# Performance work log

Hardware: AMD Instinct MI355X
Metric: run time of the kernel (lower is better)

Reference implementation:

```python
import jax, jax.numpy as jnp
import numpy as np

B, S, N, D, H, C, E, DG = 2, 512, 20000, 384, 3, 128, 320000, 128
NEG_SLOPE = 0.2  # PyG GATConv default


def setup_inputs() -> dict:
    key = jax.random.key(0)
    ks = jax.random.split(key, 10)
    p = lambda k, sh: jax.random.normal(k, sh, jnp.float32) * 0.02
    return dict(
        x_enc=jax.random.normal(ks[0], (B, S, D), jnp.float32),
        mask=jax.random.uniform(ks[1], (B, N), dtype=jnp.float32),
        edge_index=jax.random.randint(ks[2], (2, E), 0, N),
        Wq=p(ks[3], (N, S)), bq=jnp.zeros((N,), jnp.float32),
        Wm=p(ks[4], (D, 1)), bm=jnp.zeros((D,), jnp.float32),
        Wlin=p(ks[5], (H * C, D)),
        att_src=p(ks[6], (H, C)), att_dst=p(ks[7], (H, C)),
        bias_gat=jnp.zeros((H * C,), jnp.float32),
        Wproj=p(ks[8], (S, N)), bproj=jnp.zeros((S,), jnp.float32),
        Wtemp=p(ks[9], (DG, H * C)), btemp=jnp.zeros((DG,), jnp.float32),
    )


def reference(x_enc, mask, edge_index, Wq, bq, Wm, bm, Wlin, att_src, att_dst,
              bias_gat, Wproj, bproj, Wtemp, btemp):
    # q = query_proj(x_enc.permute(0,2,1)).permute(0,2,1)  -> [B, N, D]
    q = jnp.einsum('bsd,ns->bnd', x_enc, Wq) + bq[None, :, None]
    # mask_proj: Linear(1, D) on mask[..., None]  -> [B, N, D]
    mask_embed = mask[..., None] * Wm[:, 0] + bm
    x = (q + mask_embed).reshape(B * N, D)

    # batch edge_index with per-graph node offsets, then add self-loops (PyG default)
    offs = (jnp.arange(B, dtype=edge_index.dtype) * N)[:, None]
    src = (edge_index[0][None, :] + offs).reshape(-1)
    dst = (edge_index[1][None, :] + offs).reshape(-1)
    loops = jnp.arange(B * N, dtype=edge_index.dtype)
    src = jnp.concatenate([src, loops])
    dst = jnp.concatenate([dst, loops])

    # GATConv: shared linear, per-head attention
    xp = (x @ Wlin.T).reshape(B * N, H, C)                  # [BN, H, C]
    a_src = jnp.einsum('nhc,hc->nh', xp, att_src)           # [BN, H]
    a_dst = jnp.einsum('nhc,hc->nh', xp, att_dst)
    e = jax.nn.leaky_relu(a_src[src] + a_dst[dst], NEG_SLOPE)  # [Etot, H]
    # segment-softmax over incoming edges of each destination node
    emax = jax.ops.segment_max(e, dst, num_segments=B * N)
    ee = jnp.exp(e - emax[dst])
    denom = jax.ops.segment_sum(ee, dst, num_segments=B * N)
    alpha = ee / denom[dst]                                  # [Etot, H]
    out = jax.ops.segment_sum(xp[src] * alpha[..., None], dst, num_segments=B * N)
    out = out.reshape(B, N, H * C) + bias_gat                # concat heads + bias

    # dropout is identity in eval
    # project: Linear(N, S) over node dim -> [B, S, H*C]
    out = jnp.einsum('bnf,sn->bsf', out, Wproj) + bproj[None, :, None]
    # temp_project: Linear(H*C, d_graph)
    out = out @ Wtemp.T + btemp
    return out
```

## Files before the change

### kernel.cpp

```cpp
#include <hip/hip_runtime.h>
#include <hip/hip_bf16.h>
#include <cstdint>

#define B_   2
#define S_   512
#define N_   20000
#define H_   3
#define C_   128
#define E_   320000
#define DG_  128
#define D_   384
#define BN_  (B_ * N_)
#define F_   (H_ * C_)
#define ETOT_ (B_ * E_ + BN_)

#define MPADQ 20096
#define MPADL 40064

#define PNS2 32
#define PCH2 640

using short8  = __attribute__((ext_vector_type(8))) short;
using floatx4 = __attribute__((ext_vector_type(4))) float;

__device__ __forceinline__ float b2f(unsigned short u) {
  union { unsigned int i; float f; } x; x.i = ((unsigned int)u) << 16; return x.f;
}
__device__ __forceinline__ unsigned short f2b(float f) {
  __hip_bfloat16 b = __float2bfloat16(f);
  return *reinterpret_cast<unsigned short*>(&b);
}

struct bf4 { __hip_bfloat16 a, b, c, d; };

__global__ __launch_bounds__(256) void conv_wq_kernel(const float* __restrict__ Wq,
                                                      __hip_bfloat16* __restrict__ o) {
  int idx = blockIdx.x * 256 + threadIdx.x;
  if (idx >= (MPADQ * 512) / 4) return;
  int e = idx * 4;
  int row = e >> 9;
  float4 v = make_float4(0.f, 0.f, 0.f, 0.f);
  if (row < N_) v = *(const float4*)(Wq + e);
  bf4 r{__float2bfloat16(v.x), __float2bfloat16(v.y),
        __float2bfloat16(v.z), __float2bfloat16(v.w)};
  *(bf4*)(o + e) = r;
}

__global__ __launch_bounds__(256) void conv_bf16_kernel(const float* __restrict__ W,
                                                        __hip_bfloat16* __restrict__ o,
                                                        int n4) {
  int idx = blockIdx.x * 256 + threadIdx.x;
  if (idx >= n4) return;
  int e = idx * 4;
  float4 v = *(const float4*)(W + e);
  bf4 r{__float2bfloat16(v.x), __float2bfloat16(v.y),
        __float2bfloat16(v.z), __float2bfloat16(v.w)};
  *(bf4*)(o + e) = r;
}

__global__ __launch_bounds__(256) void prep_epi_kernel(
    const float* __restrict__ Wlin, const float* __restrict__ Wm,
    const float* __restrict__ bm, const float* __restrict__ Wtemp,
    float* __restrict__ epi, float* __restrict__ swt) {
  int w = (blockIdx.x * 256 + threadIdx.x) >> 6;
  int lane = threadIdx.x & 63;
  if (w < F_) {
    float s0 = 0.f, s1 = 0.f, s2 = 0.f;
    const float* row = Wlin + (size_t)w * D_;
    for (int d = lane; d < D_; d += 64) {
      float wv = row[d];
      s0 += wv; s1 += Wm[d] * wv; s2 += bm[d] * wv;
    }
#pragma unroll
    for (int o = 32; o > 0; o >>= 1) {
      s0 += __shfl_down(s0, o); s1 += __shfl_down(s1, o); s2 += __shfl_down(s2, o);
    }
    if (lane == 0) { epi[w] = s0; epi[F_ + w] = s1; epi[2 * F_ + w] = s2; }
  } else if (w < F_ + DG_) {
    int g = w - F_;
    float s = 0.f;
    const float* row = Wtemp + (size_t)g * F_;
    for (int f = lane; f < F_; f += 64) s += row[f];
#pragma unroll
    for (int o = 32; o > 0; o >>= 1) s += __shfl_down(s, o);
    if (lane == 0) swt[g] = s;
  }
}

template <int EPI>
__global__ __launch_bounds__(256) void mfma_gemm_nt(
    const __hip_bfloat16* __restrict__ A, const __hip_bfloat16* __restrict__ Bt,
    __hip_bfloat16* __restrict__ Cout, int K, int Mvalid, int ldc,
    size_t bstrideB, size_t bstrideC,
    const float* __restrict__ bq, const float* __restrict__ mask,
    const float* __restrict__ epi) {
  const int tid = threadIdx.x;
  const int m0 = blockIdx.x * 128;
  const int n0 = blockIdx.y * 128;
  const int bz = blockIdx.z;

  const unsigned short* Ap = (const unsigned short*)A;
  const unsigned short* Bp = (const unsigned short*)(Bt + bstrideB * bz);

  __shared__ __align__(16) unsigned short As[128][40];
  __shared__ __align__(16) unsigned short Bs[128][40];

  const int wave = tid >> 6, lane = tid & 63;
  const int wm = (wave & 1) * 64, wn = (wave >> 1) * 64;
  const int lrow = lane & 15, lk = (lane >> 4) * 8;

  const int srow = tid >> 2;
  const int skoff = (tid & 3) * 8;

  floatx4 acc[4][4];
#pragma unroll
  for (int i = 0; i < 4; ++i)
#pragma unroll
    for (int j = 0; j < 4; ++j) acc[i][j] = floatx4{0.f, 0.f, 0.f, 0.f};

  for (int k0 = 0; k0 < K; k0 += 32) {
    int4 av0 = *(const int4*)(Ap + (size_t)(m0 + srow) * K + k0 + skoff);
    int4 av1 = *(const int4*)(Ap + (size_t)(m0 + 64 + srow) * K + k0 + skoff);
    int4 bv0 = *(const int4*)(Bp + (size_t)(n0 + srow) * K + k0 + skoff);
    int4 bv1 = *(const int4*)(Bp + (size_t)(n0 + 64 + srow) * K + k0 + skoff);
    __syncthreads();
    *(int4*)&As[srow][skoff] = av0;
    *(int4*)&As[64 + srow][skoff] = av1;
    *(int4*)&Bs[srow][skoff] = bv0;
    *(int4*)&Bs[64 + srow][skoff] = bv1;
    __syncthreads();
    short8 af[4], bf[4];
#pragma unroll
    for (int mt = 0; mt < 4; ++mt)
      af[mt] = *(const short8*)&As[wm + mt * 16 + lrow][lk];
#pragma unroll
    for (int nt = 0; nt < 4; ++nt)
      bf[nt] = *(const short8*)&Bs[wn + nt * 16 + lrow][lk];
#pragma unroll
    for (int mt = 0; mt < 4; ++mt)
#pragma unroll
      for (int nt = 0; nt < 4; ++nt)
        acc[mt][nt] = __builtin_amdgcn_mfma_f32_16x16x32_bf16(af[mt], bf[nt],
                                                              acc[mt][nt], 0, 0, 0);
  }

  __hip_bfloat16* Cb = Cout + bstrideC * bz;
#pragma unroll
  for (int mt = 0; mt < 4; ++mt) {
#pragma unroll
    for (int r = 0; r < 4; ++r) {
      int rg = m0 + wm + mt * 16 + (lane >> 4) * 4 + r;
      if (rg < Mvalid) {
        float bqv = 0.f, mkv = 0.f;
        if (EPI) {
          bqv = bq[rg];
          mkv = mask[bz * N_ + rg];
        }
#pragma unroll
        for (int nt = 0; nt < 4; ++nt) {
          int cg = n0 + wn + nt * 16 + lrow;
          float v = acc[mt][nt][r];
          if (EPI) v += bqv * epi[cg] + mkv * epi[F_ + cg] + epi[2 * F_ + cg];
          Cb[(size_t)rg * ldc + cg] = __float2bfloat16(v);
        }
      }
    }
  }
}

__global__ __launch_bounds__(256) void gemm_gn(
    const __hip_bfloat16* __restrict__ A, const __hip_bfloat16* __restrict__ Bt,
    __hip_bfloat16* __restrict__ gnT) {
  const int tid = threadIdx.x;
  const int m0 = blockIdx.x * 128;

  const unsigned short* Ap = (const unsigned short*)A;
  const unsigned short* Bp = (const unsigned short*)Bt;

  __shared__ __align__(16) unsigned short As[128][40];
  __shared__ __align__(16) unsigned short Bs[128][40];

  const int wave = tid >> 6, lane = tid & 63;
  const int wm = (wave & 1) * 64, wn = (wave >> 1) * 64;
  const int lrow = lane & 15, lk = (lane >> 4) * 8;
  const int srow = tid >> 2;
  const int skoff = (tid & 3) * 8;

  floatx4 acc[4][4];
#pragma unroll
  for (int i = 0; i < 4; ++i)
#pragma unroll
    for (int j = 0; j < 4; ++j) acc[i][j] = floatx4{0.f, 0.f, 0.f, 0.f};

  for (int k0 = 0; k0 < F_; k0 += 32) {
    int4 av0 = *(const int4*)(Ap + (size_t)(m0 + srow) * F_ + k0 + skoff);
    int4 av1 = *(const int4*)(Ap + (size_t)(m0 + 64 + srow) * F_ + k0 + skoff);
    int4 bv0 = *(const int4*)(Bp + (size_t)(srow) * F_ + k0 + skoff);
    int4 bv1 = *(const int4*)(Bp + (size_t)(64 + srow) * F_ + k0 + skoff);
    __syncthreads();
    *(int4*)&As[srow][skoff] = av0;
    *(int4*)&As[64 + srow][skoff] = av1;
    *(int4*)&Bs[srow][skoff] = bv0;
    *(int4*)&Bs[64 + srow][skoff] = bv1;
    __syncthreads();
    short8 af[4], bf[4];
#pragma unroll
    for (int mt = 0; mt < 4; ++mt)
      af[mt] = *(const short8*)&As[wm + mt * 16 + lrow][lk];
#pragma unroll
    for (int nt = 0; nt < 4; ++nt)
      bf[nt] = *(const short8*)&Bs[wn + nt * 16 + lrow][lk];
#pragma unroll
    for (int mt = 0; mt < 4; ++mt)
#pragma unroll
      for (int nt = 0; nt < 4; ++nt)
        acc[mt][nt] = __builtin_amdgcn_mfma_f32_16x16x32_bf16(af[mt], bf[nt],
                                                              acc[mt][nt], 0, 0, 0);
  }

#pragma unroll
  for (int mt = 0; mt < 4; ++mt) {
    int rg0 = m0 + wm + mt * 16 + (lane >> 4) * 4;
    if (rg0 < BN_) {
      int b = (rg0 >= N_) ? 1 : 0;
      int n = rg0 - b * N_;
#pragma unroll
      for (int nt = 0; nt < 4; ++nt) {
        int cg = wn + nt * 16 + lrow;
        ushort4 o;
        o.x = f2b(acc[mt][nt][0]); o.y = f2b(acc[mt][nt][1]);
        o.z = f2b(acc[mt][nt][2]); o.w = f2b(acc[mt][nt][3]);
        *(ushort4*)((unsigned short*)gnT + (size_t)b * DG_ * N_ + (size_t)cg * N_ + n) = o;
      }
    }
  }
}

__global__ __launch_bounds__(256) void gemm_proj2(
    const __hip_bfloat16* __restrict__ A, const __hip_bfloat16* __restrict__ Bt,
    float* __restrict__ Ppart) {
  const int tid = threadIdx.x;
  const int m0 = blockIdx.x * 128;
  const int bz = blockIdx.z;
  const int b = bz / PNS2, ks = bz - b * PNS2;
  const int kbeg = ks * PCH2;
  const int kend = (kbeg + PCH2 < N_) ? (kbeg + PCH2) : N_;

  const unsigned short* Ap = (const unsigned short*)A;
  const unsigned short* Bp = (const unsigned short*)(Bt + (size_t)b * DG_ * N_);

  __shared__ __align__(16) unsigned short As[128][40];
  __shared__ __align__(16) unsigned short Bs[128][40];

  const int wave = tid >> 6, lane = tid & 63;
  const int wm = (wave & 1) * 64, wn = (wave >> 1) * 64;
  const int lrow = lane & 15, lk = (lane >> 4) * 8;
  const int srow = tid >> 2;
  const int skoff = (tid & 3) * 8;

  floatx4 acc[4][4];
#pragma unroll
  for (int i = 0; i < 4; ++i)
#pragma unroll
    for (int j = 0; j < 4; ++j) acc[i][j] = floatx4{0.f, 0.f, 0.f, 0.f};

  for (int k0 = kbeg; k0 < kend; k0 += 32) {
    int4 av0 = *(const int4*)(Ap + (size_t)(m0 + srow) * N_ + k0 + skoff);
    int4 av1 = *(const int4*)(Ap + (size_t)(m0 + 64 + srow) * N_ + k0 + skoff);
    int4 bv0 = *(const int4*)(Bp + (size_t)(srow) * N_ + k0 + skoff);
    int4 bv1 = *(const int4*)(Bp + (size_t)(64 + srow) * N_ + k0 + skoff);
    __syncthreads();
    *(int4*)&As[srow][skoff] = av0;
    *(int4*)&As[64 + srow][skoff] = av1;
    *(int4*)&Bs[srow][skoff] = bv0;
    *(int4*)&Bs[64 + srow][skoff] = bv1;
    __syncthreads();
    short8 af[4], bf[4];
#pragma unroll
    for (int mt = 0; mt < 4; ++mt)
      af[mt] = *(const short8*)&As[wm + mt * 16 + lrow][lk];
#pragma unroll
    for (int nt = 0; nt < 4; ++nt)
      bf[nt] = *(const short8*)&Bs[wn + nt * 16 + lrow][lk];
#pragma unroll
    for (int mt = 0; mt < 4; ++mt)
#pragma unroll
      for (int nt = 0; nt < 4; ++nt)
        acc[mt][nt] = __builtin_amdgcn_mfma_f32_16x16x32_bf16(af[mt], bf[nt],
                                                              acc[mt][nt], 0, 0, 0);
  }

  float* Pp = Ppart + (size_t)bz * S_ * DG_;
#pragma unroll
  for (int mt = 0; mt < 4; ++mt) {
#pragma unroll
    for (int r = 0; r < 4; ++r) {
      int rg = m0 + wm + mt * 16 + (lane >> 4) * 4 + r;
#pragma unroll
      for (int nt = 0; nt < 4; ++nt) {
        int cg = wn + nt * 16 + lrow;
        Pp[(size_t)rg * DG_ + cg] = acc[mt][nt][r];
      }
    }
  }
}

__global__ __launch_bounds__(256) void att_kernel(
    const __hip_bfloat16* __restrict__ xp, const float* __restrict__ att_src,
    const float* __restrict__ att_dst, float* __restrict__ a_src,
    float* __restrict__ a_dst) {
  int gid = blockIdx.x * blockDim.x + threadIdx.x;
  int wid = gid >> 6;
  int lane = threadIdx.x & 63;
  if (wid >= BN_ * H_) return;
  int i = wid / H_, h = wid - i * H_;
  const __hip_bfloat16* row = xp + (size_t)i * F_ + h * C_;
  const float* as = att_src + h * C_;
  const float* ad = att_dst + h * C_;
  float v0 = __bfloat162float(row[lane]), v1 = __bfloat162float(row[lane + 64]);
  float s1 = v0 * as[lane] + v1 * as[lane + 64];
  float s2 = v0 * ad[lane] + v1 * ad[lane + 64];
#pragma unroll
  for (int off = 32; off > 0; off >>= 1) {
    s1 += __shfl_down(s1, off);
    s2 += __shfl_down(s2, off);
  }
  if (lane == 0) {
    a_src[i * H_ + h] = s1;
    a_dst[i * H_ + h] = s2;
  }
}

__global__ __launch_bounds__(256) void count_kernel(const int* __restrict__ ei,
                                                    int* __restrict__ counts,
                                                    int* __restrict__ rank) {
  int idx = blockIdx.x * blockDim.x + threadIdx.x;
  if (idx >= 2 * E_) return;
  int b = (idx >= E_) ? 1 : 0;
  int e = idx - b * E_;
  int d = ei[E_ + e];
  rank[idx] = atomicAdd(&counts[b * N_ + d], 1);
}

__global__ __launch_bounds__(1024) void scan_kernel(const int* __restrict__ counts,
                                                    int* __restrict__ offs) {
  __shared__ int wsum[16];
  __shared__ int carry;
  int t = threadIdx.x, wave = t >> 6, lane = t & 63;
  if (t == 0) carry = 0;
  __syncthreads();
  for (int base = 0; base < BN_; base += 1024) {
    int i = base + t;
    int v = (i < BN_) ? (counts[i] + 1) : 0;
    int x = v;
#pragma unroll
    for (int o = 1; o < 64; o <<= 1) {
      int y = __shfl_up(x, o);
      if (lane >= o) x += y;
    }
    if (lane == 63) wsum[wave] = x;
    __syncthreads();
    int c = carry;
    if (wave == 0) {
      int w = (lane < 16) ? wsum[lane] : 0;
#pragma unroll
      for (int o = 1; o < 16; o <<= 1) {
        int y = __shfl_up(w, o);
        if (lane >= o) w += y;
      }
      if (lane < 16) wsum[lane] = w;
    }
    __syncthreads();
    int woff = (wave == 0) ? 0 : wsum[wave - 1];
    int excl = c + woff + x - v;
    if (i < BN_) offs[i] = excl;
    int total = wsum[15];
    __syncthreads();
    if (t == 0) carry = c + total;
  }
}

__global__ __launch_bounds__(256) void fill_kernel(
    const int* __restrict__ ei, const int* __restrict__ rank,
    const int* __restrict__ offs, const int* __restrict__ counts,
    int* __restrict__ col) {
  int idx = blockIdx.x * blockDim.x + threadIdx.x;
  if (idx >= ETOT_) return;
  if (idx < 2 * E_) {
    int b = (idx >= E_) ? 1 : 0;
    int e = idx - b * E_;
    int sg = b * N_ + ei[e];
    int dg = b * N_ + ei[E_ + e];
    col[offs[dg] + rank[idx]] = sg;
  } else {
    int i = idx - 2 * E_;
    col[offs[i] + counts[i]] = i;
  }
}

__global__ __launch_bounds__(256) void denom_kernel(
    const int* __restrict__ offs, const int* __restrict__ counts,
    const int* __restrict__ col, const float* __restrict__ a_src,
    const float* __restrict__ a_dst, float4* __restrict__ rden4) {
  int i = (blockIdx.x * 256 + threadIdx.x) >> 6;
  int lane = threadIdx.x & 63;
  if (i >= BN_) return;
  int beg = offs[i], nE = counts[i] + 1;
  float ad0 = a_dst[i * 3 + 0], ad1 = a_dst[i * 3 + 1], ad2 = a_dst[i * 3 + 2];
  float d0 = 0.f, d1 = 0.f, d2 = 0.f;
  for (int j = lane; j < nE; j += 64) {
    int s = col[beg + j];
    float e0 = a_src[s * 3 + 0] + ad0;
    float e1 = a_src[s * 3 + 1] + ad1;
    float e2 = a_src[s * 3 + 2] + ad2;
    e0 = (e0 > 0.f) ? e0 : 0.2f * e0;
    e1 = (e1 > 0.f) ? e1 : 0.2f * e1;
    e2 = (e2 > 0.f) ? e2 : 0.2f * e2;
    d0 += __expf(e0); d1 += __expf(e1); d2 += __expf(e2);
  }
#pragma unroll
  for (int o = 32; o > 0; o >>= 1) {
    d0 += __shfl_down(d0, o);
    d1 += __shfl_down(d1, o);
    d2 += __shfl_down(d2, o);
  }
  if (lane == 0) rden4[i] = make_float4(1.0f / d0, 1.0f / d1, 1.0f / d2, 0.f);
}

#define ACHK 32
__global__ __launch_bounds__(128) void agg_kernel(
    const int* __restrict__ offs, const int* __restrict__ counts,
    const int* __restrict__ col, const float* __restrict__ a_src,
    const float* __restrict__ a_dst, const float4* __restrict__ rden4,
    const __hip_bfloat16* __restrict__ xp,
    const float* __restrict__ bias_gat, __hip_bfloat16* __restrict__ out) {
  int i = blockIdx.x;
  int t = threadIdx.x;
  int beg = offs[i];
  int nE = counts[i] + 1;
  __shared__ int scol[ACHK];
  __shared__ float sexp[ACHK][4];

  const ushort4* xp4 = (const ushort4*)xp;
  int h = t >> 5;
  float ax = 0.f, ay = 0.f, az = 0.f, aw = 0.f;
  float ad0 = 0.f, ad1 = 0.f, ad2 = 0.f;
  if (t >= 96) {
    ad0 = a_dst[i * 3 + 0]; ad1 = a_dst[i * 3 + 1]; ad2 = a_dst[i * 3 + 2];
  }

  for (int c0 = 0; c0 < nE; c0 += ACHK) {
    int cn = min(ACHK, nE - c0);
    __syncthreads();
    int ts = t - 96;
    if (ts >= 0 && ts < cn) {
      int s = col[beg + c0 + ts];
      scol[ts] = s;
      float e0 = a_src[s * 3 + 0] + ad0;
      float e1 = a_src[s * 3 + 1] + ad1;
      float e2 = a_src[s * 3 + 2] + ad2;
      e0 = (e0 > 0.f) ? e0 : 0.2f * e0;
      e1 = (e1 > 0.f) ? e1 : 0.2f * e1;
      e2 = (e2 > 0.f) ? e2 : 0.2f * e2;
      sexp[ts][0] = __expf(e0);
      sexp[ts][1] = __expf(e1);
      sexp[ts][2] = __expf(e2);
    }
    __syncthreads();
    if (t < 96) {
      int j = 0;
      for (; j + 4 <= cn; j += 4) {
        int s0 = scol[j + 0], s1 = scol[j + 1], s2 = scol[j + 2], s3 = scol[j + 3];
        ushort4 v0 = xp4[(size_t)s0 * 96 + t];
        ushort4 v1 = xp4[(size_t)s1 * 96 + t];
        ushort4 v2 = xp4[(size_t)s2 * 96 + t];
        ushort4 v3 = xp4[(size_t)s3 * 96 + t];
        float w0 = sexp[j + 0][h], w1 = sexp[j + 1][h];
        float w2 = sexp[j + 2][h], w3 = sexp[j + 3][h];
        ax = fmaf(w0, b2f(v0.x), ax); ay = fmaf(w0, b2f(v0.y), ay);
        az = fmaf(w0, b2f(v0.z), az); aw = fmaf(w0, b2f(v0.w), aw);
        ax = fmaf(w1, b2f(v1.x), ax); ay = fmaf(w1, b2f(v1.y), ay);
        az = fmaf(w1, b2f(v1.z), az); aw = fmaf(w1, b2f(v1.w), aw);
        ax = fmaf(w2, b2f(v2.x), ax); ay = fmaf(w2, b2f(v2.y), ay);
        az = fmaf(w2, b2f(v2.z), az); aw = fmaf(w2, b2f(v2.w), aw);
        ax = fmaf(w3, b2f(v3.x), ax); ay = fmaf(w3, b2f(v3.y), ay);
        az = fmaf(w3, b2f(v3.z), az); aw = fmaf(w3, b2f(v3.w), aw);
      }
      for (; j < cn; ++j) {
        int s0 = scol[j];
        ushort4 v0 = xp4[(size_t)s0 * 96 + t];
        float w0 = sexp[j][h];
        ax = fmaf(w0, b2f(v0.x), ax); ay = fmaf(w0, b2f(v0.y), ay);
        az = fmaf(w0, b2f(v0.z), az); aw = fmaf(w0, b2f(v0.w), aw);
      }
    }
  }
  if (t < 96) {
    float4 rd = rden4[i];
    float r = (h == 0) ? rd.x : ((h == 1) ? rd.y : rd.z);
    const float4 bg = *(const float4*)(bias_gat + t * 4);
    ushort4 o;
    o.x = f2b(ax * r + bg.x);
    o.y = f2b(ay * r + bg.y);
    o.z = f2b(az * r + bg.z);
    o.w = f2b(aw * r + bg.w);
    *(ushort4*)((unsigned short*)out + (size_t)i * F_ + t * 4) = o;
  }
}

__global__ __launch_bounds__(128) void final_kernel(
    const float* __restrict__ Ppart, const float* __restrict__ bproj,
    const float* __restrict__ swt, const float* __restrict__ btemp,
    float* __restrict__ out) {
  int bs = blockIdx.x;
  int b = bs >> 9;
  int s = bs & (S_ - 1);
  int g = threadIdx.x;
  float acc = btemp[g] + bproj[s] * swt[g];
  const float* pp = Ppart + ((size_t)b * PNS2 * S_ + s) * DG_ + g;
  for (int ns = 0; ns < PNS2; ++ns) acc += pp[(size_t)ns * S_ * DG_];
  out[(size_t)bs * DG_ + g] = acc;
}

extern "C" void kernel_launch(void* const* d_in, const int* in_sizes, int n_in,
                              void* d_out, int out_size, void* d_ws, size_t ws_size,
                              hipStream_t stream) {
  const float* x_enc   = (const float*)d_in[0];
  const float* mask    = (const float*)d_in[1];
  const int*   ei      = (const int*)d_in[2];
  const float* Wq      = (const float*)d_in[3];
  const float* bq      = (const float*)d_in[4];
  const float* Wm      = (const float*)d_in[5];
  const float* bm      = (const float*)d_in[6];
  const float* Wlin    = (const float*)d_in[7];
  const float* att_src = (const float*)d_in[8];
  const float* att_dst = (const float*)d_in[9];
  const float* bias_gat= (const float*)d_in[10];
  const float* Wproj   = (const float*)d_in[11];
  const float* bproj   = (const float*)d_in[12];
  const float* Wtemp   = (const float*)d_in[13];
  const float* btemp   = (const float*)d_in[14];
  float* outp = (float*)d_out;

  char* ws = (char*)d_ws;
  size_t off = 0;
  auto alloc = [&](size_t bytes) {
    char* p = ws + off;
    off = (off + bytes + 255) & ~(size_t)255;
    return p;
  };

  const size_t GNT_OFF = (size_t)B_ * PNS2 * S_ * DG_ * 4;
  char* regionA = alloc(GNT_OFF + (size_t)B_ * DG_ * N_ * 2);
  __hip_bfloat16* Wq_b = (__hip_bfloat16*)regionA;
  float* Ppart = (float*)regionA;
  __hip_bfloat16* gnT  = (__hip_bfloat16*)(regionA + GNT_OFF);

  __hip_bfloat16* xeB    = (__hip_bfloat16*)alloc((size_t)B_ * S_ * D_ * 2);
  __hip_bfloat16* yT     = (__hip_bfloat16*)alloc((size_t)B_ * F_ * S_ * 2);
  __hip_bfloat16* xp     = (__hip_bfloat16*)alloc((size_t)BN_ * F_ * 2);
  __hip_bfloat16* gat    = (__hip_bfloat16*)alloc((size_t)MPADL * F_ * 2);
  __hip_bfloat16* WlinB  = (__hip_bfloat16*)alloc((size_t)F_ * D_ * 2);
  __hip_bfloat16* WprojB = (__hip_bfloat16*)alloc((size_t)S_ * N_ * 2);
  __hip_bfloat16* WtempB = (__hip_bfloat16*)alloc((size_t)DG_ * F_ * 2);
  float* epi   = (float*)alloc((size_t)3 * F_ * 4);
  float* swt   = (float*)alloc((size_t)DG_ * 4);
  float* a_src = (float*)alloc((size_t)BN_ * H_ * 4);
  float* a_dst = (float*)alloc((size_t)BN_ * H_ * 4);
  int* counts  = (int*)alloc((size_t)BN_ * 4);
  int* offsb   = (int*)alloc((size_t)BN_ * 4);
  int* rank    = (int*)alloc((size_t)2 * E_ * 4);
  int* col     = (int*)alloc((size_t)ETOT_ * 4);
  float4* rden4 = (float4*)alloc((size_t)BN_ * 16);
  if (off > ws_size) return;

  hipMemsetAsync(counts, 0, (size_t)BN_ * 4, stream);
  hipMemsetAsync(gat + (size_t)BN_ * F_, 0, (size_t)(MPADL - BN_) * F_ * 2, stream);

  count_kernel<<<(2 * E_ + 255) / 256, 256, 0, stream>>>(ei, counts, rank);
  scan_kernel<<<1, 1024, 0, stream>>>(counts, offsb);
  fill_kernel<<<(ETOT_ + 255) / 256, 256, 0, stream>>>(ei, rank, offsb, counts, col);

  conv_wq_kernel<<<(MPADQ * S_ / 4 + 255) / 256, 256, 0, stream>>>(Wq, Wq_b);
  conv_bf16_kernel<<<(B_ * S_ * D_ / 4 + 255) / 256, 256, 0, stream>>>(
      x_enc, xeB, B_ * S_ * D_ / 4);
  conv_bf16_kernel<<<(F_ * D_ / 4 + 255) / 256, 256, 0, stream>>>(Wlin, WlinB, F_ * D_ / 4);
  conv_bf16_kernel<<<(S_ * N_ / 4 + 255) / 256, 256, 0, stream>>>(Wproj, WprojB, S_ * N_ / 4);
  conv_bf16_kernel<<<(DG_ * F_ / 4 + 255) / 256, 256, 0, stream>>>(Wtemp, WtempB, DG_ * F_ / 4);
  prep_epi_kernel<<<((F_ + DG_) * 64) / 256, 256, 0, stream>>>(Wlin, Wm, bm, Wtemp, epi, swt);

  mfma_gemm_nt<0><<<dim3(F_ / 128, S_ / 128, B_), 256, 0, stream>>>(
      WlinB, xeB, yT, D_, F_, S_, (size_t)S_ * D_, (size_t)F_ * S_,
      nullptr, nullptr, nullptr);
  mfma_gemm_nt<1><<<dim3(MPADQ / 128, F_ / 128, B_), 256, 0, stream>>>(
      Wq_b, yT, xp, S_, N_, F_, (size_t)F_ * S_, (size_t)N_ * F_,
      bq, mask, epi);

  att_kernel<<<(BN_ * H_ + 3) / 4, 256, 0, stream>>>(xp, att_src, att_dst, a_src, a_dst);
  denom_kernel<<<BN_ / 4, 256, 0, stream>>>(offsb, counts, col, a_src, a_dst, rden4);
  agg_kernel<<<BN_, 128, 0, stream>>>(offsb, counts, col, a_src, a_dst, rden4,
                                      xp, bias_gat, gat);

  gemm_gn<<<dim3(MPADL / 128, 1, 1), 256, 0, stream>>>(gat, WtempB, gnT);
  gemm_proj2<<<dim3(S_ / 128, 1, B_ * PNS2), 256, 0, stream>>>(WprojB, gnT, Ppart);
  final_kernel<<<B_ * S_, 128, 0, stream>>>(Ppart, bproj, swt, btemp, outp);
}
```

Before: 429.3 us.

## Parallelize scan, fuse bf16 conversions, precompute edge exps for aggregation

```diff
diff --git a/kernel.cpp b/kernel.cpp
--- a/kernel.cpp
+++ b/kernel.cpp
@@ -33,29 +33,49 @@
 
 struct bf4 { __hip_bfloat16 a, b, c, d; };
 
-__global__ __launch_bounds__(256) void conv_wq_kernel(const float* __restrict__ Wq,
-                                                      __hip_bfloat16* __restrict__ o) {
-  int idx = blockIdx.x * 256 + threadIdx.x;
-  if (idx >= (MPADQ * 512) / 4) return;
-  int e = idx * 4;
-  int row = e >> 9;
-  float4 v = make_float4(0.f, 0.f, 0.f, 0.f);
-  if (row < N_) v = *(const float4*)(Wq + e);
+#define NWQ4 ((MPADQ * 512) / 4)
+#define NXE4 ((B_ * S_ * D_) / 4)
+#define NWL4 ((F_ * D_) / 4)
+#define NWP4 ((S_ * N_) / 4)
+#define NWT4 ((DG_ * F_) / 4)
+#define NCV0 NWQ4
+#define NCV1 (NCV0 + NXE4)
+#define NCV2 (NCV1 + NWL4)
+#define NCV3 (NCV2 + NWP4)
+#define NCV4 (NCV3 + NWT4)
+
+__device__ __forceinline__ void cv4(const float* __restrict__ src,
+                                    __hip_bfloat16* __restrict__ dst, int e) {
+  float4 v = *(const float4*)(src + e);
   bf4 r{__float2bfloat16(v.x), __float2bfloat16(v.y),
         __float2bfloat16(v.z), __float2bfloat16(v.w)};
-  *(bf4*)(o + e) = r;
-}
-
-__global__ __launch_bounds__(256) void conv_bf16_kernel(const float* __restrict__ W,
-                                                        __hip_bfloat16* __restrict__ o,
-                                                        int n4) {
+  *(bf4*)(dst + e) = r;
+}
+
+__global__ __launch_bounds__(256) void conv_all_kernel(
+    const float* __restrict__ Wq,    __hip_bfloat16* __restrict__ WqB,
+    const float* __restrict__ xe,    __hip_bfloat16* __restrict__ xeB,
+    const float* __restrict__ Wlin,  __hip_bfloat16* __restrict__ WlinB,
+    const float* __restrict__ Wproj, __hip_bfloat16* __restrict__ WprojB,
+    const float* __restrict__ Wtemp, __hip_bfloat16* __restrict__ WtempB) {
   int idx = blockIdx.x * 256 + threadIdx.x;
-  if (idx >= n4) return;
-  int e = idx * 4;
-  float4 v = *(const float4*)(W + e);
-  bf4 r{__float2bfloat16(v.x), __float2bfloat16(v.y),
-        __float2bfloat16(v.z), __float2bfloat16(v.w)};
-  *(bf4*)(o + e) = r;
+  if (idx < NCV0) {
+    int e = idx * 4;
+    int row = e >> 9;
+    float4 v = make_float4(0.f, 0.f, 0.f, 0.f);
+    if (row < N_) v = *(const float4*)(Wq + e);
+    bf4 r{__float2bfloat16(v.x), __float2bfloat16(v.y),
+          __float2bfloat16(v.z), __float2bfloat16(v.w)};
+    *(bf4*)(WqB + e) = r;
+  } else if (idx < NCV1) {
+    cv4(xe, xeB, (idx - NCV0) * 4);
+  } else if (idx < NCV2) {
+    cv4(Wlin, WlinB, (idx - NCV1) * 4);
+  } else if (idx < NCV3) {
+    cv4(Wproj, WprojB, (idx - NCV2) * 4);
+  } else if (idx < NCV4) {
+    cv4(Wtemp, WtempB, (idx - NCV3) * 4);
+  }
 }
 
 __global__ __launch_bounds__(256) void prep_epi_kernel(
@@ -342,42 +362,54 @@
   rank[idx] = atomicAdd(&counts[b * N_ + d], 1);
 }
 
-__global__ __launch_bounds__(1024) void scan_kernel(const int* __restrict__ counts,
-                                                    int* __restrict__ offs) {
+#define SCB 1024
+#define NSCB ((BN_ + SCB - 1) / SCB)
+__global__ __launch_bounds__(1024) void scan1_kernel(const int* __restrict__ counts,
+                                                     int* __restrict__ offs,
+                                                     int* __restrict__ btot) {
   __shared__ int wsum[16];
-  __shared__ int carry;
   int t = threadIdx.x, wave = t >> 6, lane = t & 63;
-  if (t == 0) carry = 0;
+  int i = blockIdx.x * SCB + t;
+  int v = (i < BN_) ? (counts[i] + 1) : 0;
+  int x = v;
+#pragma unroll
+  for (int o = 1; o < 64; o <<= 1) {
+    int y = __shfl_up(x, o);
+    if (lane >= o) x += y;
+  }
+  if (lane == 63) wsum[wave] = x;
   __syncthreads();
-  for (int base = 0; base < BN_; base += 1024) {
-    int i = base + t;
-    int v = (i < BN_) ? (counts[i] + 1) : 0;
-    int x = v;
-#pragma unroll
-    for (int o = 1; o < 64; o <<= 1) {
-      int y = __shfl_up(x, o);
-      if (lane >= o) x += y;
+  if (wave == 0) {
+    int w = (lane < 16) ? wsum[lane] : 0;
+#pragma unroll
+    for (int o = 1; o < 16; o <<= 1) {
+      int y = __shfl_up(w, o);
+      if (lane >= o) w += y;
     }
-    if (lane == 63) wsum[wave] = x;
-    __syncthreads();
-    int c = carry;
-    if (wave == 0) {
-      int w = (lane < 16) ? wsum[lane] : 0;
-#pragma unroll
-      for (int o = 1; o < 16; o <<= 1) {
-        int y = __shfl_up(w, o);
-        if (lane >= o) w += y;
-      }
-      if (lane < 16) wsum[lane] = w;
-    }
-    __syncthreads();
-    int woff = (wave == 0) ? 0 : wsum[wave - 1];
-    int excl = c + woff + x - v;
-    if (i < BN_) offs[i] = excl;
-    int total = wsum[15];
-    __syncthreads();
-    if (t == 0) carry = c + total;
-  }
+    if (lane < 16) wsum[lane] = w;
+  }
+  __syncthreads();
+  int woff = (wave == 0) ? 0 : wsum[wave - 1];
+  if (i < BN_) offs[i] = woff + x - v;
+  if (t == 0) btot[blockIdx.x] = wsum[15];
+}
+
+__global__ __launch_bounds__(64) void scan2_kernel(int* __restrict__ btot) {
+  int lane = threadIdx.x;
+  int v = (lane < NSCB) ? btot[lane] : 0;
+  int x = v;
+#pragma unroll
+  for (int o = 1; o < 64; o <<= 1) {
+    int y = __shfl_up(x, o);
+    if (lane >= o) x += y;
+  }
+  if (lane < NSCB) btot[lane] = x - v;
+}
+
+__global__ __launch_bounds__(256) void scan3_kernel(int* __restrict__ offs,
+                                                    const int* __restrict__ btot) {
+  int i = blockIdx.x * 256 + threadIdx.x;
+  if (i < BN_) offs[i] += btot[i >> 10];
 }
 
 __global__ __launch_bounds__(256) void fill_kernel(
@@ -401,7 +433,8 @@
 __global__ __launch_bounds__(256) void denom_kernel(
     const int* __restrict__ offs, const int* __restrict__ counts,
     const int* __restrict__ col, const float* __restrict__ a_src,
-    const float* __restrict__ a_dst, float4* __restrict__ rden4) {
+    const float* __restrict__ a_dst, float4* __restrict__ rden4,
+    float4* __restrict__ sexp4) {
   int i = (blockIdx.x * 256 + threadIdx.x) >> 6;
   int lane = threadIdx.x & 63;
   if (i >= BN_) return;
@@ -416,7 +449,9 @@
     e0 = (e0 > 0.f) ? e0 : 0.2f * e0;
     e1 = (e1 > 0.f) ? e1 : 0.2f * e1;
     e2 = (e2 > 0.f) ? e2 : 0.2f * e2;
-    d0 += __expf(e0); d1 += __expf(e1); d2 += __expf(e2);
+    float x0 = __expf(e0), x1 = __expf(e1), x2 = __expf(e2);
+    sexp4[beg + j] = make_float4(x0, x1, x2, 0.f);
+    d0 += x0; d1 += x1; d2 += x2;
   }
 #pragma unroll
   for (int o = 32; o > 0; o >>= 1) {
@@ -427,85 +462,59 @@
   if (lane == 0) rden4[i] = make_float4(1.0f / d0, 1.0f / d1, 1.0f / d2, 0.f);
 }
 
-#define ACHK 32
 __global__ __launch_bounds__(128) void agg_kernel(
     const int* __restrict__ offs, const int* __restrict__ counts,
-    const int* __restrict__ col, const float* __restrict__ a_src,
-    const float* __restrict__ a_dst, const float4* __restrict__ rden4,
-    const __hip_bfloat16* __restrict__ xp,
+    const int* __restrict__ col, const float* __restrict__ sexpw,
+    const float4* __restrict__ rden4, const __hip_bfloat16* __restrict__ xp,
     const float* __restrict__ bias_gat, __hip_bfloat16* __restrict__ out) {
   int i = blockIdx.x;
   int t = threadIdx.x;
+  if (t >= 96) return;
   int beg = offs[i];
   int nE = counts[i] + 1;
-  __shared__ int scol[ACHK];
-  __shared__ float sexp[ACHK][4];
 
   const ushort4* xp4 = (const ushort4*)xp;
   int h = t >> 5;
   float ax = 0.f, ay = 0.f, az = 0.f, aw = 0.f;
-  float ad0 = 0.f, ad1 = 0.f, ad2 = 0.f;
-  if (t >= 96) {
-    ad0 = a_dst[i * 3 + 0]; ad1 = a_dst[i * 3 + 1]; ad2 = a_dst[i * 3 + 2];
-  }
-
-  for (int c0 = 0; c0 < nE; c0 += ACHK) {
-    int cn = min(ACHK, nE - c0);
-    __syncthreads();
-    int ts = t - 96;
-    if (ts >= 0 && ts < cn) {
-      int s = col[beg + c0 + ts];
-      scol[ts] = s;
-      float e0 = a_src[s * 3 + 0] + ad0;
-      float e1 = a_src[s * 3 + 1] + ad1;
-      float e2 = a_src[s * 3 + 2] + ad2;
-      e0 = (e0 > 0.f) ? e0 : 0.2f * e0;
-      e1 = (e1 > 0.f) ? e1 : 0.2f * e1;
-      e2 = (e2 > 0.f) ? e2 : 0.2f * e2;
-      sexp[ts][0] = __expf(e0);
-      sexp[ts][1] = __expf(e1);
-      sexp[ts][2] = __expf(e2);
-    }
-    __syncthreads();
-    if (t < 96) {
-      int j = 0;
-      for (; j + 4 <= cn; j += 4) {
-        int s0 = scol[j + 0], s1 = scol[j + 1], s2 = scol[j + 2], s3 = scol[j + 3];
-        ushort4 v0 = xp4[(size_t)s0 * 96 + t];
-        ushort4 v1 = xp4[(size_t)s1 * 96 + t];
-        ushort4 v2 = xp4[(size_t)s2 * 96 + t];
-        ushort4 v3 = xp4[(size_t)s3 * 96 + t];
-        float w0 = sexp[j + 0][h], w1 = sexp[j + 1][h];
-        float w2 = sexp[j + 2][h], w3 = sexp[j + 3][h];
-        ax = fmaf(w0, b2f(v0.x), ax); ay = fmaf(w0, b2f(v0.y), ay);
-        az = fmaf(w0, b2f(v0.z), az); aw = fmaf(w0, b2f(v0.w), aw);
-        ax = fmaf(w1, b2f(v1.x), ax); ay = fmaf(w1, b2f(v1.y), ay);
-        az = fmaf(w1, b2f(v1.z), az); aw = fmaf(w1, b2f(v1.w), aw);
-        ax = fmaf(w2, b2f(v2.x), ax); ay = fmaf(w2, b2f(v2.y), ay);
-        az = fmaf(w2, b2f(v2.z), az); aw = fmaf(w2, b2f(v2.w), aw);
-        ax = fmaf(w3, b2f(v3.x), ax); ay = fmaf(w3, b2f(v3.y), ay);
-        az = fmaf(w3, b2f(v3.z), az); aw = fmaf(w3, b2f(v3.w), aw);
-      }
-      for (; j < cn; ++j) {
-        int s0 = scol[j];
-        ushort4 v0 = xp4[(size_t)s0 * 96 + t];
-        float w0 = sexp[j][h];
-        ax = fmaf(w0, b2f(v0.x), ax); ay = fmaf(w0, b2f(v0.y), ay);
-        az = fmaf(w0, b2f(v0.z), az); aw = fmaf(w0, b2f(v0.w), aw);
-      }
-    }
-  }
-  if (t < 96) {
-    float4 rd = rden4[i];
-    float r = (h == 0) ? rd.x : ((h == 1) ? rd.y : rd.z);
-    const float4 bg = *(const float4*)(bias_gat + t * 4);
-    ushort4 o;
-    o.x = f2b(ax * r + bg.x);
-    o.y = f2b(ay * r + bg.y);
-    o.z = f2b(az * r + bg.z);
-    o.w = f2b(aw * r + bg.w);
-    *(ushort4*)((unsigned short*)out + (size_t)i * F_ + t * 4) = o;
-  }
+
+  int j = 0;
+  for (; j + 4 <= nE; j += 4) {
+    int s0 = col[beg + j + 0], s1 = col[beg + j + 1];
+    int s2 = col[beg + j + 2], s3 = col[beg + j + 3];
+    float w0 = sexpw[(beg + j + 0) * 4 + h];
+    float w1 = sexpw[(beg + j + 1) * 4 + h];
+    float w2 = sexpw[(beg + j + 2) * 4 + h];
+    float w3 = sexpw[(beg + j + 3) * 4 + h];
+    ushort4 v0 = xp4[(size_t)s0 * 96 + t];
+    ushort4 v1 = xp4[(size_t)s1 * 96 + t];
+    ushort4 v2 = xp4[(size_t)s2 * 96 + t];
+    ushort4 v3 = xp4[(size_t)s3 * 96 + t];
+    ax = fmaf(w0, b2f(v0.x), ax); ay = fmaf(w0, b2f(v0.y), ay);
+    az = fmaf(w0, b2f(v0.z), az); aw = fmaf(w0, b2f(v0.w), aw);
+    ax = fmaf(w1, b2f(v1.x), ax); ay = fmaf(w1, b2f(v1.y), ay);
+    az = fmaf(w1, b2f(v1.z), az); aw = fmaf(w1, b2f(v1.w), aw);
+    ax = fmaf(w2, b2f(v2.x), ax); ay = fmaf(w2, b2f(v2.y), ay);
+    az = fmaf(w2, b2f(v2.z), az); aw = fmaf(w2, b2f(v2.w), aw);
+    ax = fmaf(w3, b2f(v3.x), ax); ay = fmaf(w3, b2f(v3.y), ay);
+    az = fmaf(w3, b2f(v3.z), az); aw = fmaf(w3, b2f(v3.w), aw);
+  }
+  for (; j < nE; ++j) {
+    int s0 = col[beg + j];
+    float w0 = sexpw[(beg + j) * 4 + h];
+    ushort4 v0 = xp4[(size_t)s0 * 96 + t];
+    ax = fmaf(w0, b2f(v0.x), ax); ay = fmaf(w0, b2f(v0.y), ay);
+    az = fmaf(w0, b2f(v0.z), az); aw = fmaf(w0, b2f(v0.w), aw);
+  }
+
+  float4 rd = rden4[i];
+  float r = (h == 0) ? rd.x : ((h == 1) ? rd.y : rd.z);
+  const float4 bg = *(const float4*)(bias_gat + t * 4);
+  ushort4 o;
+  o.x = f2b(ax * r + bg.x);
+  o.y = f2b(ay * r + bg.y);
+  o.z = f2b(az * r + bg.z);
+  o.w = f2b(aw * r + bg.w);
+  *(ushort4*)((unsigned short*)out + (size_t)i * F_ + t * 4) = o;
 }
 
 __global__ __launch_bounds__(128) void final_kernel(
@@ -571,22 +580,22 @@
   int* offsb   = (int*)alloc((size_t)BN_ * 4);
   int* rank    = (int*)alloc((size_t)2 * E_ * 4);
   int* col     = (int*)alloc((size_t)ETOT_ * 4);
+  int* btot    = (int*)alloc((size_t)NSCB * 4);
   float4* rden4 = (float4*)alloc((size_t)BN_ * 16);
+  float4* sexp4 = (float4*)alloc((size_t)ETOT_ * 16);
   if (off > ws_size) return;
 
   hipMemsetAsync(counts, 0, (size_t)BN_ * 4, stream);
   hipMemsetAsync(gat + (size_t)BN_ * F_, 0, (size_t)(MPADL - BN_) * F_ * 2, stream);
 
   count_kernel<<<(2 * E_ + 255) / 256, 256, 0, stream>>>(ei, counts, rank);
-  scan_kernel<<<1, 1024, 0, stream>>>(counts, offsb);
+  scan1_kernel<<<NSCB, SCB, 0, stream>>>(counts, offsb, btot);
+  scan2_kernel<<<1, 64, 0, stream>>>(btot);
+  scan3_kernel<<<(BN_ + 255) / 256, 256, 0, stream>>>(offsb, btot);
   fill_kernel<<<(ETOT_ + 255) / 256, 256, 0, stream>>>(ei, rank, offsb, counts, col);
 
-  conv_wq_kernel<<<(MPADQ * S_ / 4 + 255) / 256, 256, 0, stream>>>(Wq, Wq_b);
-  conv_bf16_kernel<<<(B_ * S_ * D_ / 4 + 255) / 256, 256, 0, stream>>>(
-      x_enc, xeB, B_ * S_ * D_ / 4);
-  conv_bf16_kernel<<<(F_ * D_ / 4 + 255) / 256, 256, 0, stream>>>(Wlin, WlinB, F_ * D_ / 4);
-  conv_bf16_kernel<<<(S_ * N_ / 4 + 255) / 256, 256, 0, stream>>>(Wproj, WprojB, S_ * N_ / 4);
-  conv_bf16_kernel<<<(DG_ * F_ / 4 + 255) / 256, 256, 0, stream>>>(Wtemp, WtempB, DG_ * F_ / 4);
+  conv_all_kernel<<<(NCV4 + 255) / 256, 256, 0, stream>>>(
+      Wq, Wq_b, x_enc, xeB, Wlin, WlinB, Wproj, WprojB, Wtemp, WtempB);
   prep_epi_kernel<<<((F_ + DG_) * 64) / 256, 256, 0, stream>>>(Wlin, Wm, bm, Wtemp, epi, swt);
 
   mfma_gemm_nt<0><<<dim3(F_ / 128, S_ / 128, B_), 256, 0, stream>>>(
@@ -597,8 +606,8 @@
       bq, mask, epi);
 
   att_kernel<<<(BN_ * H_ + 3) / 4, 256, 0, stream>>>(xp, att_src, att_dst, a_src, a_dst);
-  denom_kernel<<<BN_ / 4, 256, 0, stream>>>(offsb, counts, col, a_src, a_dst, rden4);
-  agg_kernel<<<BN_, 128, 0, stream>>>(offsb, counts, col, a_src, a_dst, rden4,
+  denom_kernel<<<BN_ / 4, 256, 0, stream>>>(offsb, counts, col, a_src, a_dst, rden4, sexp4);
+  agg_kernel<<<BN_, 128, 0, stream>>>(offsb, counts, col, (const float*)sexp4, rden4,
                                       xp, bias_gat, gat);
 
   gemm_gn<<<dim3(MPADL / 128, 1, 1), 256, 0, stream>>>(gat, WtempB, gnT);
```

Result: faster. 387.1 us (-9.8%).
